# Optimization experiments

Hardware: AMD Instinct MI355X
Metric: run time of the kernel (lower is better)

Reference implementation:

```python
import jax, jax.numpy as jnp
import numpy as np

N_HEADS = 16
MAX_LEN = 1024


def setup_inputs() -> dict:
    key = jax.random.key(0)
    ks = jax.random.split(key, 6)
    B, T, C = 4, 1024, 1024
    scale = 0.02
    return {
        "x": jax.random.normal(ks[0], (B, T, C), dtype=jnp.float32),
        "qkv_w": jax.random.normal(ks[1], (3 * C, C), dtype=jnp.float32) * scale,
        "qkv_b": jax.random.normal(ks[2], (3 * C,), dtype=jnp.float32) * scale,
        "proj_w": jax.random.normal(ks[3], (C, C), dtype=jnp.float32) * scale,
        "proj_b": jax.random.normal(ks[4], (C,), dtype=jnp.float32) * scale,
        "rel_pos_emb": jax.random.normal(ks[5], (2 * MAX_LEN - 1, C), dtype=jnp.float32) * scale,
    }


def reference(x, qkv_w, qkv_b, proj_w, proj_b, rel_pos_emb):
    B, T, C = x.shape
    H = N_HEADS
    D = C // H
    # QKV projection: (B,T,3C) -> (3,B,H,T,D)
    qkv = (x @ qkv_w.T + qkv_b).reshape(B, T, 3, H, D)
    qkv = jnp.transpose(qkv, (2, 0, 3, 1, 4))
    q, k, v = qkv[0], qkv[1], qkv[2]
    # scores: (B,H,T,T)
    att = jnp.einsum("bhtd,bhsd->bhts", q, k) / np.sqrt(D).astype(np.float32)
    # Relative position bias: gather-then-sum == sum-then-gather over head_dim.
    # Pre-reduce table to (2*max_len-1, H) to avoid materializing (T,T,C).
    table = rel_pos_emb.reshape(2 * MAX_LEN - 1, H, D).sum(axis=-1)  # (2L-1, H)
    pos = jnp.arange(T)
    rel_idx = pos[:, None] - pos[None, :] + (MAX_LEN - 1)  # (T,T)
    bias = jnp.transpose(table[rel_idx], (2, 0, 1))  # (H,T,T)
    att = att + bias[None]
    # causal mask: positions j > i masked to -inf
    causal = pos[None, :] > pos[:, None]  # (T,T) True above diagonal
    att = jnp.where(causal[None, None], -jnp.inf, att)
    att = jax.nn.softmax(att, axis=-1)
    out = jnp.einsum("bhts,bhsd->bhtd", att, v)  # (B,H,T,D)
    out = jnp.transpose(out, (0, 2, 1, 3)).reshape(B, T, C)
    return out @ proj_w.T + proj_b
```

## Files before the change

### kernel.cpp

```cpp
#include <hip/hip_runtime.h>
#include <hip/hip_bf16.h>


typedef __bf16 bf16x8 __attribute__((ext_vector_type(8)));
typedef float f32x4 __attribute__((ext_vector_type(4)));

__device__ __forceinline__ float bf2f(unsigned short u) {
    return __uint_as_float(((unsigned)u) << 16);
}
__device__ __forceinline__ unsigned short f2bf(float f) {
    __hip_bfloat16 h = __float2bfloat16(f);
    return *reinterpret_cast<unsigned short*>(&h);
}
__device__ __forceinline__ int4 cvt8(float4 a, float4 b) {
    union { unsigned short s[8]; int4 v; } u;
    u.s[0] = f2bf(a.x); u.s[1] = f2bf(a.y); u.s[2] = f2bf(a.z); u.s[3] = f2bf(a.w);
    u.s[4] = f2bf(b.x); u.s[5] = f2bf(b.y); u.s[6] = f2bf(b.z); u.s[7] = f2bf(b.w);
    return u.v;
}

__global__ __launch_bounds__(256) void table_reduce(const float* __restrict__ rel,
                                                    float* __restrict__ table) {
    const int p = blockIdx.x;
    const int tid = threadIdx.x, lane = tid & 63, wave = tid >> 6;
    const float* r = rel + (size_t)p * 1024;
    float s[4];
#pragma unroll
    for (int k = 0; k < 4; ++k) s[k] = r[tid + 256 * k];
#pragma unroll
    for (int k = 0; k < 4; ++k) {
        float v = s[k];
        for (int o = 32; o; o >>= 1) v += __shfl_xor(v, o, 64);
        if (lane == 0) table[p * 16 + wave + 4 * k] = v;
    }
}

template <int EPI, bool AF32>
__global__ __launch_bounds__(512) void gemm_bt(const void* __restrict__ Ain,
                                               const float* __restrict__ Bf,
                                               const float* __restrict__ bias,
                                               unsigned short* __restrict__ outb,
                                               float* __restrict__ outf,
                                               int M, int N, int K) {
    __shared__ __attribute__((aligned(16))) unsigned short As[128 * 40];
    __shared__ __attribute__((aligned(16))) unsigned short Bs[128 * 40];
    const int bm = blockIdx.x * 128, bn = blockIdx.y * 128;
    const int tid = threadIdx.x, lane = tid & 63, wave = tid >> 6;
    const int wr = wave & 1, wc = wave >> 1;
    const int quad = lane >> 4, lm = lane & 15;

    const int srow = tid >> 2;
    const int scol = (tid & 3) * 8;
    const float* ApF          = (const float*)Ain + (size_t)(bm + srow) * K + scol;
    const unsigned short* ApH = (const unsigned short*)Ain + (size_t)(bm + srow) * K + scol;
    const float* BpF          = Bf + (size_t)(bn + srow) * K + scol;
    unsigned short* AsW = &As[srow * 40 + scol];
    unsigned short* BsW = &Bs[srow * 40 + scol];

    f32x4 acc[4][2];
#pragma unroll
    for (int r = 0; r < 4; ++r)
#pragma unroll
        for (int c = 0; c < 2; ++c) acc[r][c] = (f32x4){0.f, 0.f, 0.f, 0.f};

    float4 paf0, paf1, pbf0, pbf1;
    int4 pah;
    if (AF32) {
        paf0 = *(const float4*)(ApF);
        paf1 = *(const float4*)(ApF + 4);
    } else {
        pah = *(const int4*)(ApH);
    }
    pbf0 = *(const float4*)(BpF);
    pbf1 = *(const float4*)(BpF + 4);

    for (int kk = 0; kk < K; kk += 32) {
        *(int4*)(AsW) = AF32 ? cvt8(paf0, paf1) : pah;
        *(int4*)(BsW) = cvt8(pbf0, pbf1);
        __syncthreads();

        if (kk + 32 < K) {
            if (AF32) {
                paf0 = *(const float4*)(ApF + kk + 32);
                paf1 = *(const float4*)(ApF + kk + 36);
            } else {
                pah = *(const int4*)(ApH + kk + 32);
            }
            pbf0 = *(const float4*)(BpF + kk + 32);
            pbf1 = *(const float4*)(BpF + kk + 36);
        }

        bf16x8 af[4], bfr[2];
#pragma unroll
        for (int r = 0; r < 4; ++r)
            af[r] = *(const bf16x8*)(&As[(64 * wr + 16 * r + lm) * 40 + quad * 8]);
#pragma unroll
        for (int c = 0; c < 2; ++c)
            bfr[c] = *(const bf16x8*)(&Bs[(32 * wc + 16 * c + lm) * 40 + quad * 8]);
#pragma unroll
        for (int r = 0; r < 4; ++r)
#pragma unroll
            for (int c = 0; c < 2; ++c)
                acc[r][c] = __builtin_amdgcn_mfma_f32_16x16x32_bf16(af[r], bfr[c], acc[r][c], 0, 0, 0);
        __syncthreads();
    }

#pragma unroll
    for (int r = 0; r < 4; ++r)
#pragma unroll
        for (int c = 0; c < 2; ++c)
#pragma unroll
            for (int i = 0; i < 4; ++i) {
                const int row = bm + 64 * wr + 16 * r + quad * 4 + i;
                const int col = bn + 32 * wc + 16 * c + lm;
                const float v = acc[r][c][i] + bias[col];
                if (EPI == 0) {
                    const int b = row >> 10, t = row & 1023;
                    const int s3 = col >> 10, rem = col & 1023;
                    const int h = rem >> 6, d = rem & 63;
                    const size_t base = (((size_t)s3 * 4 + b) * 16 + h) * 65536;
                    const size_t off = base + (s3 == 2 ? (size_t)d * 1024 + t
                                                       : (size_t)t * 64 + d);
                    outb[off] = f2bf(v);
                } else {
                    outf[(size_t)row * N + col] = v;
                }
            }
}

__global__ __launch_bounds__(512) void attn_mfma(const unsigned short* __restrict__ qkvb,
                                                 const float* __restrict__ table,
                                                 unsigned short* __restrict__ y) {
    const int bh = blockIdx.x, b = bh >> 4, h = bh & 15;
    const int qb = (7 - blockIdx.y) * 128;
    const int tid = threadIdx.x, lane = tid & 63, wave = tid >> 6;
    const int quad = lane >> 4, lm = lane & 15;

    __shared__ __attribute__((aligned(16))) unsigned short Ks[64][72];
    __shared__ __attribute__((aligned(16))) unsigned short Vs[64][72];
    __shared__ __attribute__((aligned(16))) unsigned short Ps[8][16][72];
    __shared__ float tb[1280];

    const unsigned short* Qg  = qkvb + ((size_t)(b)*16 + h) * 65536;
    const unsigned short* Kg  = qkvb + ((size_t)(4 + b)*16 + h) * 65536;
    const unsigned short* Vtg = qkvb + ((size_t)(8 + b)*16 + h) * 65536;

    const bf16x8 qf0 = *(const bf16x8*)(Qg + (size_t)(qb + wave * 16 + lm) * 64 + quad * 8);
    const bf16x8 qf1 = *(const bf16x8*)(Qg + (size_t)(qb + wave * 16 + lm) * 64 + 32 + quad * 8);

    const int tbn = qb + 255;
    for (int i = tid; i < tbn; i += 512) tb[i] = table[(896 + i) * 16 + h];

    f32x4 oacc[4];
#pragma unroll
    for (int nb = 0; nb < 4; ++nb) oacc[nb] = (f32x4){0.f, 0.f, 0.f, 0.f};
    float mi = -1e30f, li = 0.f;

    const int r0 = tid >> 3, c0 = (tid & 7) * 8;
    int4 pk = *(const int4*)(Kg + (size_t)r0 * 64 + c0);
    int4 pv = *(const int4*)(Vtg + (size_t)r0 * 1024 + c0);

    const int q = qb + wave * 16 + lm;
    const int ktiles = qb / 64 + 2;
    for (int kt = 0; kt < ktiles; ++kt) {
        *(int4*)&Ks[r0][c0] = pk;
        *(int4*)&Vs[r0][c0] = pv;
        __syncthreads();
        if (kt + 1 < ktiles) {
            pk = *(const int4*)(Kg + (size_t)((kt + 1) * 64 + r0) * 64 + c0);
            pv = *(const int4*)(Vtg + (size_t)r0 * 1024 + (kt + 1) * 64 + c0);
        }

        f32x4 s[4];
#pragma unroll
        for (int nb = 0; nb < 4; ++nb) {
            bf16x8 k0 = *(const bf16x8*)(&Ks[nb * 16 + lm][quad * 8]);
            bf16x8 k1 = *(const bf16x8*)(&Ks[nb * 16 + lm][32 + quad * 8]);
            s[nb] = (f32x4){0.f, 0.f, 0.f, 0.f};
            s[nb] = __builtin_amdgcn_mfma_f32_16x16x32_bf16(k0, qf0, s[nb], 0, 0, 0);
            s[nb] = __builtin_amdgcn_mfma_f32_16x16x32_bf16(k1, qf1, s[nb], 0, 0, 0);
        }

        const int jb0 = kt * 64 + quad * 4;
#pragma unroll
        for (int nb = 0; nb < 4; ++nb)
#pragma unroll
            for (int i = 0; i < 4; ++i) {
                const int j = jb0 + nb * 16 + i;
                const float v = fmaf(s[nb][i], 0.125f, tb[q - j + 127]);
                s[nb][i] = (j <= q) ? v : -1e30f;
            }

        float mx = -1e30f;
#pragma unroll
        for (int nb = 0; nb < 4; ++nb)
#pragma unroll
            for (int i = 0; i < 4; ++i) mx = fmaxf(mx, s[nb][i]);
        mx = fmaxf(mx, __shfl_xor(mx, 16, 64));
        mx = fmaxf(mx, __shfl_xor(mx, 32, 64));
        const float mnew = fmaxf(mi, mx);
        const float alpha = __expf(mi - mnew);
        mi = mnew;
#pragma unroll
        for (int nb = 0; nb < 4; ++nb)
#pragma unroll
            for (int i = 0; i < 4; ++i) s[nb][i] = __expf(s[nb][i] - mnew);
        float ps = 0.f;
#pragma unroll
        for (int nb = 0; nb < 4; ++nb)
            ps += (s[nb][0] + s[nb][1]) + (s[nb][2] + s[nb][3]);
        ps += __shfl_xor(ps, 16, 64);
        ps += __shfl_xor(ps, 32, 64);
        li = li * alpha + ps;

#pragma unroll
        for (int nb = 0; nb < 4; ++nb) {
            union { unsigned short u[4]; int2 v; } p4;
            p4.u[0] = f2bf(s[nb][0]);
            p4.u[1] = f2bf(s[nb][1]);
            p4.u[2] = f2bf(s[nb][2]);
            p4.u[3] = f2bf(s[nb][3]);
            *(int2*)(&Ps[wave][lm][nb * 16 + quad * 4]) = p4.v;
        }

        float alr[4];
#pragma unroll
        for (int i = 0; i < 4; ++i) alr[i] = __shfl(alpha, quad * 4 + i, 64);
#pragma unroll
        for (int nb = 0; nb < 4; ++nb)
#pragma unroll
            for (int i = 0; i < 4; ++i) oacc[nb][i] *= alr[i];

        const bf16x8 p0 = *(const bf16x8*)(&Ps[wave][lm][quad * 8]);
        const bf16x8 p1 = *(const bf16x8*)(&Ps[wave][lm][32 + quad * 8]);
#pragma unroll
        for (int nb = 0; nb < 4; ++nb) {
            bf16x8 v0 = *(const bf16x8*)(&Vs[nb * 16 + lm][quad * 8]);
            bf16x8 v1 = *(const bf16x8*)(&Vs[nb * 16 + lm][32 + quad * 8]);
            oacc[nb] = __builtin_amdgcn_mfma_f32_16x16x32_bf16(p0, v0, oacc[nb], 0, 0, 0);
            oacc[nb] = __builtin_amdgcn_mfma_f32_16x16x32_bf16(p1, v1, oacc[nb], 0, 0, 0);
        }
        __syncthreads();
    }

    const float linv = 1.0f / li;
    float invr[4];
#pragma unroll
    for (int i = 0; i < 4; ++i) invr[i] = __shfl(linv, quad * 4 + i, 64);
#pragma unroll
    for (int nb = 0; nb < 4; ++nb)
#pragma unroll
        for (int i = 0; i < 4; ++i) {
            const int qq = qb + wave * 16 + quad * 4 + i;
            const int d = nb * 16 + lm;
            y[((size_t)(b * 1024 + qq)) * 1024 + h * 64 + d] = f2bf(oacc[nb][i] * invr[i]);
        }
}

extern "C" void kernel_launch(void* const* d_in, const int* in_sizes, int n_in,
                              void* d_out, int out_size, void* d_ws, size_t ws_size,
                              hipStream_t stream) {
    const float* x      = (const float*)d_in[0];
    const float* qkv_w  = (const float*)d_in[1];
    const float* qkv_b  = (const float*)d_in[2];
    const float* proj_w = (const float*)d_in[3];
    const float* proj_b = (const float*)d_in[4];
    const float* rel    = (const float*)d_in[5];
    float* out = (float*)d_out;

    char* ws = (char*)d_ws;
    float* table         = (float*)(ws + 16777216);
    unsigned short* qkvb = (unsigned short*)(ws + 16908288);
    unsigned short* yb   = (unsigned short*)(ws + 42074112);

    table_reduce<<<2047, 256, 0, stream>>>(rel, table);
    gemm_bt<0, true><<<dim3(32, 24), 512, 0, stream>>>(x, qkv_w, qkv_b, qkvb, nullptr,
                                                       4096, 3072, 1024);
    attn_mfma<<<dim3(64, 8), 512, 0, stream>>>(qkvb, table, yb);
    gemm_bt<1, false><<<dim3(32, 8), 512, 0, stream>>>(yb, proj_w, proj_b, nullptr, out,
                                                       4096, 1024, 1024);
}
```

Before: 193.1 us.

## Fold table reduction into QKV GEMM grid and widen attention KV tiles

Removes the separate table_reduce launch by adding an extra row of blocks to the QKV GEMM grid that performs the relative-position table reduction, saving one kernel launch. The attention kernel now stages 128 keys/values per shared-memory tile, processed as two 64-key halves, which halves the number of barrier-separated iterations, and it skips halves lying entirely above the causal diagonal for a wave. This raises shared-memory use and register pressure for the prefetch buffers.

```diff
diff --git a/kernel.cpp b/kernel.cpp
--- a/kernel.cpp
+++ b/kernel.cpp
@@ -17,22 +17,6 @@
     u.s[0] = f2bf(a.x); u.s[1] = f2bf(a.y); u.s[2] = f2bf(a.z); u.s[3] = f2bf(a.w);
     u.s[4] = f2bf(b.x); u.s[5] = f2bf(b.y); u.s[6] = f2bf(b.z); u.s[7] = f2bf(b.w);
     return u.v;
-}
-
-__global__ __launch_bounds__(256) void table_reduce(const float* __restrict__ rel,
-                                                    float* __restrict__ table) {
-    const int p = blockIdx.x;
-    const int tid = threadIdx.x, lane = tid & 63, wave = tid >> 6;
-    const float* r = rel + (size_t)p * 1024;
-    float s[4];
-#pragma unroll
-    for (int k = 0; k < 4; ++k) s[k] = r[tid + 256 * k];
-#pragma unroll
-    for (int k = 0; k < 4; ++k) {
-        float v = s[k];
-        for (int o = 32; o; o >>= 1) v += __shfl_xor(v, o, 64);
-        if (lane == 0) table[p * 16 + wave + 4 * k] = v;
-    }
 }
 
 template <int EPI, bool AF32>
@@ -41,11 +25,34 @@
                                                const float* __restrict__ bias,
                                                unsigned short* __restrict__ outb,
                                                float* __restrict__ outf,
+                                               const float* __restrict__ rel,
+                                               float* __restrict__ table,
                                                int M, int N, int K) {
+    const int tid = threadIdx.x;
+    if (EPI == 0 && blockIdx.y == 24) {
+        const int g = tid >> 8;
+        const int t = tid & 255;
+        const int lane = t & 63, wv = t >> 6;
+        for (int it = 0; it < 32; ++it) {
+            const int p = blockIdx.x * 64 + it * 2 + g;
+            if (p < 2047) {
+                const float* r = rel + (size_t)p * 1024;
+                float s0 = r[t], s1 = r[t + 256], s2 = r[t + 512], s3 = r[t + 768];
+#pragma unroll
+                for (int k = 0; k < 4; ++k) {
+                    float v = (k == 0) ? s0 : (k == 1) ? s1 : (k == 2) ? s2 : s3;
+                    for (int o = 32; o; o >>= 1) v += __shfl_xor(v, o, 64);
+                    if (lane == 0) table[p * 16 + wv + 4 * k] = v;
+                }
+            }
+        }
+        return;
+    }
+
     __shared__ __attribute__((aligned(16))) unsigned short As[128 * 40];
     __shared__ __attribute__((aligned(16))) unsigned short Bs[128 * 40];
     const int bm = blockIdx.x * 128, bn = blockIdx.y * 128;
-    const int tid = threadIdx.x, lane = tid & 63, wave = tid >> 6;
+    const int lane = tid & 63, wave = tid >> 6;
     const int wr = wave & 1, wc = wave >> 1;
     const int quad = lane >> 4, lm = lane & 15;
 
@@ -136,8 +143,8 @@
     const int tid = threadIdx.x, lane = tid & 63, wave = tid >> 6;
     const int quad = lane >> 4, lm = lane & 15;
 
-    __shared__ __attribute__((aligned(16))) unsigned short Ks[64][72];
-    __shared__ __attribute__((aligned(16))) unsigned short Vs[64][72];
+    __shared__ __attribute__((aligned(16))) unsigned short Ks[128][72];
+    __shared__ __attribute__((aligned(16))) unsigned short Vs[64][136];
     __shared__ __attribute__((aligned(16))) unsigned short Ps[8][16][72];
     __shared__ float tb[1280];
 
@@ -156,89 +163,104 @@
     for (int nb = 0; nb < 4; ++nb) oacc[nb] = (f32x4){0.f, 0.f, 0.f, 0.f};
     float mi = -1e30f, li = 0.f;
 
-    const int r0 = tid >> 3, c0 = (tid & 7) * 8;
-    int4 pk = *(const int4*)(Kg + (size_t)r0 * 64 + c0);
-    int4 pv = *(const int4*)(Vtg + (size_t)r0 * 1024 + c0);
+    const int kr = tid >> 2, kc = (tid & 3) * 16;
+    const int vr = tid >> 3, vc = (tid & 7) * 8;
+    int4 pk0 = *(const int4*)(Kg + (size_t)kr * 64 + kc);
+    int4 pk1 = *(const int4*)(Kg + (size_t)kr * 64 + kc + 8);
+    int4 pv0 = *(const int4*)(Vtg + (size_t)vr * 1024 + vc);
+    int4 pv1 = *(const int4*)(Vtg + (size_t)vr * 1024 + vc + 64);
 
     const int q = qb + wave * 16 + lm;
-    const int ktiles = qb / 64 + 2;
-    for (int kt = 0; kt < ktiles; ++kt) {
-        *(int4*)&Ks[r0][c0] = pk;
-        *(int4*)&Vs[r0][c0] = pv;
+    const int qwave_hi = qb + wave * 16 + 15;
+    const int ktpairs = qb / 128 + 1;
+    for (int kt2 = 0; kt2 < ktpairs; ++kt2) {
+        *(int4*)&Ks[kr][kc]     = pk0;
+        *(int4*)&Ks[kr][kc + 8] = pk1;
+        *(int4*)&Vs[vr][vc]      = pv0;
+        *(int4*)&Vs[vr][vc + 64] = pv1;
         __syncthreads();
-        if (kt + 1 < ktiles) {
-            pk = *(const int4*)(Kg + (size_t)((kt + 1) * 64 + r0) * 64 + c0);
-            pv = *(const int4*)(Vtg + (size_t)r0 * 1024 + (kt + 1) * 64 + c0);
-        }
-
-        f32x4 s[4];
-#pragma unroll
-        for (int nb = 0; nb < 4; ++nb) {
-            bf16x8 k0 = *(const bf16x8*)(&Ks[nb * 16 + lm][quad * 8]);
-            bf16x8 k1 = *(const bf16x8*)(&Ks[nb * 16 + lm][32 + quad * 8]);
-            s[nb] = (f32x4){0.f, 0.f, 0.f, 0.f};
-            s[nb] = __builtin_amdgcn_mfma_f32_16x16x32_bf16(k0, qf0, s[nb], 0, 0, 0);
-            s[nb] = __builtin_amdgcn_mfma_f32_16x16x32_bf16(k1, qf1, s[nb], 0, 0, 0);
-        }
-
-        const int jb0 = kt * 64 + quad * 4;
-#pragma unroll
-        for (int nb = 0; nb < 4; ++nb)
-#pragma unroll
-            for (int i = 0; i < 4; ++i) {
-                const int j = jb0 + nb * 16 + i;
-                const float v = fmaf(s[nb][i], 0.125f, tb[q - j + 127]);
-                s[nb][i] = (j <= q) ? v : -1e30f;
-            }
-
-        float mx = -1e30f;
-#pragma unroll
-        for (int nb = 0; nb < 4; ++nb)
-#pragma unroll
-            for (int i = 0; i < 4; ++i) mx = fmaxf(mx, s[nb][i]);
-        mx = fmaxf(mx, __shfl_xor(mx, 16, 64));
-        mx = fmaxf(mx, __shfl_xor(mx, 32, 64));
-        const float mnew = fmaxf(mi, mx);
-        const float alpha = __expf(mi - mnew);
-        mi = mnew;
-#pragma unroll
-        for (int nb = 0; nb < 4; ++nb)
-#pragma unroll
-            for (int i = 0; i < 4; ++i) s[nb][i] = __expf(s[nb][i] - mnew);
-        float ps = 0.f;
-#pragma unroll
-        for (int nb = 0; nb < 4; ++nb)
-            ps += (s[nb][0] + s[nb][1]) + (s[nb][2] + s[nb][3]);
-        ps += __shfl_xor(ps, 16, 64);
-        ps += __shfl_xor(ps, 32, 64);
-        li = li * alpha + ps;
-
-#pragma unroll
-        for (int nb = 0; nb < 4; ++nb) {
-            union { unsigned short u[4]; int2 v; } p4;
-            p4.u[0] = f2bf(s[nb][0]);
-            p4.u[1] = f2bf(s[nb][1]);
-            p4.u[2] = f2bf(s[nb][2]);
-            p4.u[3] = f2bf(s[nb][3]);
-            *(int2*)(&Ps[wave][lm][nb * 16 + quad * 4]) = p4.v;
-        }
-
-        float alr[4];
-#pragma unroll
-        for (int i = 0; i < 4; ++i) alr[i] = __shfl(alpha, quad * 4 + i, 64);
-#pragma unroll
-        for (int nb = 0; nb < 4; ++nb)
-#pragma unroll
-            for (int i = 0; i < 4; ++i) oacc[nb][i] *= alr[i];
-
-        const bf16x8 p0 = *(const bf16x8*)(&Ps[wave][lm][quad * 8]);
-        const bf16x8 p1 = *(const bf16x8*)(&Ps[wave][lm][32 + quad * 8]);
-#pragma unroll
-        for (int nb = 0; nb < 4; ++nb) {
-            bf16x8 v0 = *(const bf16x8*)(&Vs[nb * 16 + lm][quad * 8]);
-            bf16x8 v1 = *(const bf16x8*)(&Vs[nb * 16 + lm][32 + quad * 8]);
-            oacc[nb] = __builtin_amdgcn_mfma_f32_16x16x32_bf16(p0, v0, oacc[nb], 0, 0, 0);
-            oacc[nb] = __builtin_amdgcn_mfma_f32_16x16x32_bf16(p1, v1, oacc[nb], 0, 0, 0);
+        if (kt2 + 1 < ktpairs) {
+            const int j0n = (kt2 + 1) * 128;
+            pk0 = *(const int4*)(Kg + (size_t)(j0n + kr) * 64 + kc);
+            pk1 = *(const int4*)(Kg + (size_t)(j0n + kr) * 64 + kc + 8);
+            pv0 = *(const int4*)(Vtg + (size_t)vr * 1024 + j0n + vc);
+            pv1 = *(const int4*)(Vtg + (size_t)vr * 1024 + j0n + vc + 64);
+        }
+
+#pragma unroll
+        for (int hf = 0; hf < 2; ++hf) {
+            const int jb = kt2 * 128 + hf * 64;
+            if (qwave_hi < jb) continue;
+
+            f32x4 s[4];
+#pragma unroll
+            for (int nb = 0; nb < 4; ++nb) {
+                bf16x8 k0 = *(const bf16x8*)(&Ks[hf * 64 + nb * 16 + lm][quad * 8]);
+                bf16x8 k1 = *(const bf16x8*)(&Ks[hf * 64 + nb * 16 + lm][32 + quad * 8]);
+                s[nb] = (f32x4){0.f, 0.f, 0.f, 0.f};
+                s[nb] = __builtin_amdgcn_mfma_f32_16x16x32_bf16(k0, qf0, s[nb], 0, 0, 0);
+                s[nb] = __builtin_amdgcn_mfma_f32_16x16x32_bf16(k1, qf1, s[nb], 0, 0, 0);
+            }
+
+            const int jq0 = jb + quad * 4;
+#pragma unroll
+            for (int nb = 0; nb < 4; ++nb)
+#pragma unroll
+                for (int i = 0; i < 4; ++i) {
+                    const int j = jq0 + nb * 16 + i;
+                    const float v = fmaf(s[nb][i], 0.125f, tb[q - j + 127]);
+                    s[nb][i] = (j <= q) ? v : -1e30f;
+                }
+
+            float mx = -1e30f;
+#pragma unroll
+            for (int nb = 0; nb < 4; ++nb)
+#pragma unroll
+                for (int i = 0; i < 4; ++i) mx = fmaxf(mx, s[nb][i]);
+            mx = fmaxf(mx, __shfl_xor(mx, 16, 64));
+            mx = fmaxf(mx, __shfl_xor(mx, 32, 64));
+            const float mnew = fmaxf(mi, mx);
+            const float alpha = __expf(mi - mnew);
+            mi = mnew;
+#pragma unroll
+            for (int nb = 0; nb < 4; ++nb)
+#pragma unroll
+                for (int i = 0; i < 4; ++i) s[nb][i] = __expf(s[nb][i] - mnew);
+            float ps = 0.f;
+#pragma unroll
+            for (int nb = 0; nb < 4; ++nb)
+                ps += (s[nb][0] + s[nb][1]) + (s[nb][2] + s[nb][3]);
+            ps += __shfl_xor(ps, 16, 64);
+            ps += __shfl_xor(ps, 32, 64);
+            li = li * alpha + ps;
+
+#pragma unroll
+            for (int nb = 0; nb < 4; ++nb) {
+                union { unsigned short u[4]; int2 v; } p4;
+                p4.u[0] = f2bf(s[nb][0]);
+                p4.u[1] = f2bf(s[nb][1]);
+                p4.u[2] = f2bf(s[nb][2]);
+                p4.u[3] = f2bf(s[nb][3]);
+                *(int2*)(&Ps[wave][lm][nb * 16 + quad * 4]) = p4.v;
+            }
+
+            float alr[4];
+#pragma unroll
+            for (int i = 0; i < 4; ++i) alr[i] = __shfl(alpha, quad * 4 + i, 64);
+#pragma unroll
+            for (int nb = 0; nb < 4; ++nb)
+#pragma unroll
+                for (int i = 0; i < 4; ++i) oacc[nb][i] *= alr[i];
+
+            const bf16x8 p0 = *(const bf16x8*)(&Ps[wave][lm][quad * 8]);
+            const bf16x8 p1 = *(const bf16x8*)(&Ps[wave][lm][32 + quad * 8]);
+#pragma unroll
+            for (int nb = 0; nb < 4; ++nb) {
+                bf16x8 v0 = *(const bf16x8*)(&Vs[nb * 16 + lm][hf * 64 + quad * 8]);
+                bf16x8 v1 = *(const bf16x8*)(&Vs[nb * 16 + lm][hf * 64 + 32 + quad * 8]);
+                oacc[nb] = __builtin_amdgcn_mfma_f32_16x16x32_bf16(p0, v0, oacc[nb], 0, 0, 0);
+                oacc[nb] = __builtin_amdgcn_mfma_f32_16x16x32_bf16(p1, v1, oacc[nb], 0, 0, 0);
+            }
         }
         __syncthreads();
     }
@@ -273,10 +295,9 @@
     unsigned short* qkvb = (unsigned short*)(ws + 16908288);
     unsigned short* yb   = (unsigned short*)(ws + 42074112);
 
-    table_reduce<<<2047, 256, 0, stream>>>(rel, table);
-    gemm_bt<0, true><<<dim3(32, 24), 512, 0, stream>>>(x, qkv_w, qkv_b, qkvb, nullptr,
-                                                       4096, 3072, 1024);
+    gemm_bt<0, true><<<dim3(32, 25), 512, 0, stream>>>(x, qkv_w, qkv_b, qkvb, nullptr,
+                                                       rel, table, 4096, 3072, 1024);
     attn_mfma<<<dim3(64, 8), 512, 0, stream>>>(qkvb, table, yb);
     gemm_bt<1, false><<<dim3(32, 8), 512, 0, stream>>>(yb, proj_w, proj_b, nullptr, out,
-                                                       4096, 1024, 1024);
-}
+                                                       nullptr, nullptr, 4096, 1024, 1024);
+}
```

Result: slower. 220.1 us (+14.0%).
